# Kernel tuning notes

Measured on AMD Instinct MI355X. Metric: run time of the kernel, lower is better.

## Reference

```python
import jax, jax.numpy as jnp
import numpy as np

N_NODES = 100000
IN_DIM = 500
HID_DIM = 128
OUT_DIM = 40
N_EDGES = 1600000


def setup_inputs() -> dict:
    key = jax.random.key(0)
    k1, k2, k3, k4, k5 = jax.random.split(key, 5)
    x = jax.random.normal(k1, (N_NODES, IN_DIM), dtype=jnp.float32)
    edge_index = jax.random.randint(k2, (2, N_EDGES), 0, N_NODES, dtype=jnp.int64)
    # Glorot-style init for linear weights, zero bias (as in PyG GCNConv)
    W1 = jax.random.normal(k3, (IN_DIM, HID_DIM), dtype=jnp.float32) / np.sqrt(IN_DIM)
    b1 = jnp.zeros((HID_DIM,), dtype=jnp.float32)
    W2 = jax.random.normal(k4, (HID_DIM, OUT_DIM), dtype=jnp.float32) / np.sqrt(HID_DIM)
    b2 = jnp.zeros((OUT_DIM,), dtype=jnp.float32)
    return {"x": x, "edge_index": edge_index, "W1": W1, "b1": b1, "W2": W2, "b2": b2}


def reference(x, edge_index, W1, b1, W2, b2):
    N = x.shape[0]
    # GCNConv: add self-loops, symmetric normalization deg^-1/2 A deg^-1/2
    loops = jnp.arange(N, dtype=edge_index.dtype)
    src = jnp.concatenate([edge_index[0], loops])  # [E+N]
    dst = jnp.concatenate([edge_index[1], loops])  # [E+N]
    deg = jax.ops.segment_sum(jnp.ones_like(dst, dtype=x.dtype), dst, num_segments=N)
    dinv = jnp.where(deg > 0, jax.lax.rsqrt(deg), 0.0)
    norm = (dinv[src] * dinv[dst])[:, None]  # [E+N, 1]

    def gcn_conv(h, W, b):
        h = h @ W                              # [N, F_out] linear first (PyG order)
        msg = h[src] * norm                    # gather + scale: [E+N, F_out]
        agg = jax.ops.segment_sum(msg, dst, num_segments=N)  # scatter-add
        return agg + b

    h = jax.nn.relu(gcn_conv(x, W1, b1))
    # dropout(p=0.5) is identity in eval mode
    h = gcn_conv(h, W2, b2)
    return jax.nn.log_softmax(h, axis=1)
```

## Files before the change

### kernel.cpp

```cpp
#include <hip/hip_runtime.h>
#include <hip/hip_bf16.h>

#define IN_DIM 500
#define HID 128
#define OUTD 40
#define KPAD 512

typedef __bf16 bf16x8 __attribute__((ext_vector_type(8)));
typedef float f32x16 __attribute__((ext_vector_type(16)));

static __device__ __forceinline__ float rsqrt_acc(float x) {
  float r = rsqrtf(x);
  return r * (1.5f - 0.5f * x * r * r);
}

static __device__ __forceinline__ unsigned short bf16_of(float f) {
  __bf16 h = (__bf16)f;
  return __builtin_bit_cast(unsigned short, h);
}
static __device__ __forceinline__ float bf16_back(unsigned short u) {
  return (float)__builtin_bit_cast(__bf16, u);
}

__global__ void zero_kernel(int* __restrict__ p, int n) {
  int i = blockIdx.x * 256 + threadIdx.x;
  if (i < n) p[i] = 0;
}

__global__ void hist_kernel(const int* __restrict__ dst, int* __restrict__ deg, int E) {
  int e = blockIdx.x * 256 + threadIdx.x;
  if (e < E) atomicAdd(&deg[dst[e]], 1);
}

__global__ void dinv_kernel(const int* __restrict__ deg, float* __restrict__ dinv, int N) {
  int n = blockIdx.x * 256 + threadIdx.x;
  if (n < N) dinv[n] = rsqrt_acc((float)deg[n] + 1.0f);
}

__global__ void scan_a(const int* __restrict__ deg, int* __restrict__ partial,
                       int* __restrict__ blockSums, int N) {
  __shared__ int sums[256];
  int t = threadIdx.x;
  int base = blockIdx.x * 1024 + t * 4;
  int v0 = (base + 0) < N ? deg[base + 0] : 0;
  int v1 = (base + 1) < N ? deg[base + 1] : 0;
  int v2 = (base + 2) < N ? deg[base + 2] : 0;
  int v3 = (base + 3) < N ? deg[base + 3] : 0;
  int l0 = v0, l1 = l0 + v1, l2 = l1 + v2, l3 = l2 + v3;
  sums[t] = l3;
  __syncthreads();
  for (int o = 1; o < 256; o <<= 1) {
    int a = sums[t];
    int b = (t >= o) ? sums[t - o] : 0;
    __syncthreads();
    sums[t] = a + b;
    __syncthreads();
  }
  int excl = sums[t] - l3;
  if (t == 0) blockSums[blockIdx.x] = sums[255];
  if (base + 0 < N) partial[base + 0] = excl;
  if (base + 1 < N) partial[base + 1] = excl + l0;
  if (base + 2 < N) partial[base + 2] = excl + l1;
  if (base + 3 < N) partial[base + 3] = excl + l2;
}

__global__ void scan_b(int* __restrict__ blockSums, int nb) {
  __shared__ int s[256];
  int t = threadIdx.x;
  int orig = (t < nb) ? blockSums[t] : 0;
  s[t] = orig;
  __syncthreads();
  for (int o = 1; o < 256; o <<= 1) {
    int a = s[t];
    int b = (t >= o) ? s[t - o] : 0;
    __syncthreads();
    s[t] = a + b;
    __syncthreads();
  }
  if (t < nb) blockSums[t] = s[t] - orig;
}

__global__ void scan_c(int* __restrict__ row_ptr, const int* __restrict__ blockOff,
                       int* __restrict__ cursor, int N, int E) {
  int n = blockIdx.x * 256 + threadIdx.x;
  if (n < N) {
    int v = row_ptr[n] + blockOff[n >> 10];
    row_ptr[n] = v;
    cursor[n] = v;
  }
  if (n == 0 && blockIdx.x == 0) row_ptr[N] = E;
}

__global__ void place_kernel(const int* __restrict__ src, const int* __restrict__ dst,
                             const float* __restrict__ dinv, int* __restrict__ cursor,
                             int* __restrict__ eSrc, float* __restrict__ eW, int E) {
  int e = blockIdx.x * 256 + threadIdx.x;
  if (e < E) {
    int s = src[e], d = dst[e];
    int pos = atomicAdd(&cursor[d], 1);
    eSrc[pos] = s;
    eW[pos] = dinv[s] * dinv[d];
  }
}

__global__ void convW1_kernel(const float* __restrict__ W1, unsigned short* __restrict__ Whi,
                              unsigned short* __restrict__ Wlo) {
  int idx = blockIdx.x * 256 + threadIdx.x;
  if (idx >= HID * KPAD) return;
  int n = idx >> 9, k = idx & (KPAD - 1);
  float f = (k < IN_DIM) ? W1[(size_t)k * HID + n] : 0.f;
  unsigned short h = bf16_of(f);
  Whi[idx] = h;
  Wlo[idx] = bf16_of(f - bf16_back(h));
}

#define LSTR 40
__global__ __launch_bounds__(256) void gemm1_kernel(const float* __restrict__ X,
                                                    const unsigned short* __restrict__ Whi,
                                                    const unsigned short* __restrict__ Wlo,
                                                    float* __restrict__ H1, int N) {
  __shared__ unsigned short sAhi[128 * LSTR];
  __shared__ unsigned short sAlo[128 * LSTR];
  __shared__ unsigned short sBhi[128 * LSTR];
  __shared__ unsigned short sBlo[128 * LSTR];
  const int t = threadIdx.x;
  const int rowBase = blockIdx.x * 128;
  const int lane = t & 63;
  const int w = t >> 6;
  const int m = lane & 31;
  const int quad = lane >> 5;

  f32x16 acc[4];
#pragma unroll
  for (int i = 0; i < 4; i++) acc[i] = (f32x16)(0.f);

  const int srow = t >> 1;
  const int skoff = (t & 1) * 16;
  const bool rok = (rowBase + srow) < N;
  const float* xrow = X + (size_t)(rowBase + (rok ? srow : 0)) * IN_DIM;

  for (int k0 = 0; k0 < KPAD; k0 += 32) {
    __syncthreads();
    {
      float f[16];
      if (rok && (k0 + skoff + 16) <= IN_DIM) {
        const float4* p = (const float4*)(xrow + k0 + skoff);
        float4 v0 = p[0], v1 = p[1], v2 = p[2], v3 = p[3];
        f[0]=v0.x; f[1]=v0.y; f[2]=v0.z; f[3]=v0.w;
        f[4]=v1.x; f[5]=v1.y; f[6]=v1.z; f[7]=v1.w;
        f[8]=v2.x; f[9]=v2.y; f[10]=v2.z; f[11]=v2.w;
        f[12]=v3.x; f[13]=v3.y; f[14]=v3.z; f[15]=v3.w;
      } else {
#pragma unroll
        for (int j = 0; j < 16; j++) {
          int k = k0 + skoff + j;
          f[j] = (rok && k < IN_DIM) ? xrow[k] : 0.f;
        }
      }
#pragma unroll
      for (int g = 0; g < 4; g++) {
        ushort4 h, l;
        h.x = bf16_of(f[g*4+0]); l.x = bf16_of(f[g*4+0] - bf16_back(h.x));
        h.y = bf16_of(f[g*4+1]); l.y = bf16_of(f[g*4+1] - bf16_back(h.y));
        h.z = bf16_of(f[g*4+2]); l.z = bf16_of(f[g*4+2] - bf16_back(h.z));
        h.w = bf16_of(f[g*4+3]); l.w = bf16_of(f[g*4+3] - bf16_back(h.w));
        *(ushort4*)&sAhi[srow * LSTR + skoff + g * 4] = h;
        *(ushort4*)&sAlo[srow * LSTR + skoff + g * 4] = l;
      }
    }
    {
      const int n = srow;
      const size_t gb = (size_t)n * KPAD + k0 + skoff;
      uint4 h0 = *(const uint4*)&Whi[gb];
      uint4 h1v = *(const uint4*)&Whi[gb + 8];
      uint4 l0 = *(const uint4*)&Wlo[gb];
      uint4 l1 = *(const uint4*)&Wlo[gb + 8];
      *(uint4*)&sBhi[n * LSTR + skoff] = h0;
      *(uint4*)&sBhi[n * LSTR + skoff + 8] = h1v;
      *(uint4*)&sBlo[n * LSTR + skoff] = l0;
      *(uint4*)&sBlo[n * LSTR + skoff + 8] = l1;
    }
    __syncthreads();

#pragma unroll
    for (int sub = 0; sub < 2; sub++) {
      const int ks = sub * 16 + quad * 8;
      bf16x8 ah = *(const bf16x8*)&sAhi[(w * 32 + m) * LSTR + ks];
      bf16x8 al = *(const bf16x8*)&sAlo[(w * 32 + m) * LSTR + ks];
#pragma unroll
      for (int nt = 0; nt < 4; nt++) {
        bf16x8 bh = *(const bf16x8*)&sBhi[(nt * 32 + m) * LSTR + ks];
        bf16x8 bl = *(const bf16x8*)&sBlo[(nt * 32 + m) * LSTR + ks];
        acc[nt] = __builtin_amdgcn_mfma_f32_32x32x16_bf16(ah, bh, acc[nt], 0, 0, 0);
        acc[nt] = __builtin_amdgcn_mfma_f32_32x32x16_bf16(ah, bl, acc[nt], 0, 0, 0);
        acc[nt] = __builtin_amdgcn_mfma_f32_32x32x16_bf16(al, bh, acc[nt], 0, 0, 0);
      }
    }
  }

#pragma unroll
  for (int nt = 0; nt < 4; nt++) {
#pragma unroll
    for (int r = 0; r < 16; r++) {
      int rowin = (r & 3) + 8 * (r >> 2) + 4 * quad;
      int grow = rowBase + w * 32 + rowin;
      if (grow < N) H1[(size_t)grow * HID + nt * 32 + m] = acc[nt][r];
    }
  }
}

__global__ void agg1_kernel(const float* __restrict__ h1, const int* __restrict__ row_ptr,
                            const int* __restrict__ eSrc, const float* __restrict__ eW,
                            const float* __restrict__ dinv, const float* __restrict__ b1,
                            float* __restrict__ hrelu, int N) {
  int gid = blockIdx.x * 256 + threadIdx.x;
  int n = gid >> 5, c4 = (gid & 31) * 4;
  if (n >= N) return;
  float di = dinv[n];
  float sl = di * di;
  float4 acc = *(const float4*)&h1[(size_t)n * HID + c4];
  acc.x *= sl; acc.y *= sl; acc.z *= sl; acc.w *= sl;
  int i = row_ptr[n];
  const int s1 = row_ptr[n + 1];
  for (; i + 4 <= s1; i += 4) {
    int j0 = eSrc[i], j1 = eSrc[i + 1], j2 = eSrc[i + 2], j3 = eSrc[i + 3];
    float w0 = eW[i], w1 = eW[i + 1], w2 = eW[i + 2], w3 = eW[i + 3];
    float4 v0 = *(const float4*)&h1[(size_t)j0 * HID + c4];
    float4 v1 = *(const float4*)&h1[(size_t)j1 * HID + c4];
    float4 v2 = *(const float4*)&h1[(size_t)j2 * HID + c4];
    float4 v3 = *(const float4*)&h1[(size_t)j3 * HID + c4];
    acc.x += w0 * v0.x + w1 * v1.x + w2 * v2.x + w3 * v3.x;
    acc.y += w0 * v0.y + w1 * v1.y + w2 * v2.y + w3 * v3.y;
    acc.z += w0 * v0.z + w1 * v1.z + w2 * v2.z + w3 * v3.z;
    acc.w += w0 * v0.w + w1 * v1.w + w2 * v2.w + w3 * v3.w;
  }
  for (; i < s1; i++) {
    int j = eSrc[i];
    float w = eW[i];
    float4 v = *(const float4*)&h1[(size_t)j * HID + c4];
    acc.x += w * v.x; acc.y += w * v.y; acc.z += w * v.z; acc.w += w * v.w;
  }
  float4 bb = *(const float4*)&b1[c4];
  float4 r;
  r.x = fmaxf(acc.x + bb.x, 0.f);
  r.y = fmaxf(acc.y + bb.y, 0.f);
  r.z = fmaxf(acc.z + bb.z, 0.f);
  r.w = fmaxf(acc.w + bb.w, 0.f);
  *(float4*)&hrelu[(size_t)n * HID + c4] = r;
}

__global__ __launch_bounds__(256) void gemm2_kernel(const float* __restrict__ A,
                                                    const float* __restrict__ W2,
                                                    float* __restrict__ H2, int N) {
  __shared__ float tA[64 * 129];
  __shared__ float w2s[128 * 48];
  const int t = threadIdx.x;
  const int rowBase = blockIdx.x * 64;
  for (int idx = t; idx < 128 * 48; idx += 256) {
    int k = idx / 48, c = idx - k * 48;
    w2s[idx] = (c < OUTD) ? W2[k * OUTD + c] : 0.f;
  }
  for (int f = t; f < 2048; f += 256) {
    int row = f >> 5, c4 = (f & 31) * 4;
    float4 v = make_float4(0.f, 0.f, 0.f, 0.f);
    if (rowBase + row < N) v = *(const float4*)&A[(size_t)(rowBase + row) * HID + c4];
    tA[row * 129 + c4 + 0] = v.x;
    tA[row * 129 + c4 + 1] = v.y;
    tA[row * 129 + c4 + 2] = v.z;
    tA[row * 129 + c4 + 3] = v.w;
  }
  __syncthreads();
  const int row = t >> 2;
  const int c0 = (t & 3) * 12;
  float acc[12];
#pragma unroll
  for (int j = 0; j < 12; j++) acc[j] = 0.f;
  for (int k = 0; k < HID; k++) {
    float a = tA[row * 129 + k];
    const float* bp = &w2s[k * 48 + c0];
#pragma unroll
    for (int j = 0; j < 12; j++) acc[j] += a * bp[j];
  }
  int r = rowBase + row;
  if (r < N) {
#pragma unroll
    for (int j = 0; j < 12; j++) {
      int c = c0 + j;
      if (c < OUTD) H2[(size_t)r * OUTD + c] = acc[j];
    }
  }
}

__global__ void agg2_kernel(const float* __restrict__ h2, const int* __restrict__ row_ptr,
                            const int* __restrict__ eSrc, const float* __restrict__ eW,
                            const float* __restrict__ dinv, const float* __restrict__ b2,
                            float* __restrict__ out, int N) {
  int gid = blockIdx.x * 256 + threadIdx.x;
  int n = gid / 10;
  int c4 = (gid - n * 10) * 4;
  if (n >= N) return;
  float di = dinv[n];
  float sl = di * di;
  float4 acc = *(const float4*)&h2[(size_t)n * OUTD + c4];
  acc.x *= sl; acc.y *= sl; acc.z *= sl; acc.w *= sl;
  int i = row_ptr[n];
  const int s1 = row_ptr[n + 1];
  for (; i + 4 <= s1; i += 4) {
    int j0 = eSrc[i], j1 = eSrc[i + 1], j2 = eSrc[i + 2], j3 = eSrc[i + 3];
    float w0 = eW[i], w1 = eW[i + 1], w2 = eW[i + 2], w3 = eW[i + 3];
    float4 v0 = *(const float4*)&h2[(size_t)j0 * OUTD + c4];
    float4 v1 = *(const float4*)&h2[(size_t)j1 * OUTD + c4];
    float4 v2 = *(const float4*)&h2[(size_t)j2 * OUTD + c4];
    float4 v3 = *(const float4*)&h2[(size_t)j3 * OUTD + c4];
    acc.x += w0 * v0.x + w1 * v1.x + w2 * v2.x + w3 * v3.x;
    acc.y += w0 * v0.y + w1 * v1.y + w2 * v2.y + w3 * v3.y;
    acc.z += w0 * v0.z + w1 * v1.z + w2 * v2.z + w3 * v3.z;
    acc.w += w0 * v0.w + w1 * v1.w + w2 * v2.w + w3 * v3.w;
  }
  for (; i < s1; i++) {
    int j = eSrc[i];
    float w = eW[i];
    float4 v = *(const float4*)&h2[(size_t)j * OUTD + c4];
    acc.x += w * v.x; acc.y += w * v.y; acc.z += w * v.z; acc.w += w * v.w;
  }
  float* o = &out[(size_t)n * OUTD + c4];
  o[0] = acc.x + b2[c4 + 0];
  o[1] = acc.y + b2[c4 + 1];
  o[2] = acc.z + b2[c4 + 2];
  o[3] = acc.w + b2[c4 + 3];
}

__global__ void lsm_kernel(float* __restrict__ out, int N) {
  int n = blockIdx.x * 256 + threadIdx.x;
  if (n >= N) return;
  float* row = out + (size_t)n * OUTD;
  float v[OUTD];
  float m = -3.4e38f;
#pragma unroll
  for (int j = 0; j < OUTD; j++) {
    v[j] = row[j];
    m = fmaxf(m, v[j]);
  }
  float s = 0.f;
#pragma unroll
  for (int j = 0; j < OUTD; j++) s += expf(v[j] - m);
  float lse = m + logf(s);
#pragma unroll
  for (int j = 0; j < OUTD; j++) row[j] = v[j] - lse;
}

extern "C" void kernel_launch(void* const* d_in, const int* in_sizes, int n_in,
                              void* d_out, int out_size, void* d_ws, size_t ws_size,
                              hipStream_t stream) {
  const float* x  = (const float*)d_in[0];
  const int*   ei = (const int*)d_in[1];
  const float* W1 = (const float*)d_in[2];
  const float* b1 = (const float*)d_in[3];
  const float* W2 = (const float*)d_in[4];
  const float* b2 = (const float*)d_in[5];
  float* out = (float*)d_out;

  const int N = in_sizes[0] / IN_DIM;
  const int E = in_sizes[1] / 2;
  const int* src = ei;
  const int* dst = ei + E;

  char* wsb = (char*)d_ws;
  size_t off = 0;
  auto alloc = [&](size_t bytes) -> char* {
    char* p = wsb + off;
    off = (off + bytes + 1023) & ~(size_t)1023;
    return p;
  };
  int*   deg       = (int*)alloc((size_t)N * 4);
  float* dinv      = (float*)alloc((size_t)N * 4);
  int*   blockSums = (int*)alloc(1024);
  int*   row_ptr   = (int*)alloc((size_t)(N + 1) * 4);
  int*   cursor    = (int*)alloc((size_t)N * 4);
  int*   eSrc      = (int*)alloc((size_t)E * 4);
  float* eW        = (float*)alloc((size_t)E * 4);
  unsigned short* Whi = (unsigned short*)alloc((size_t)HID * KPAD * 2);
  unsigned short* Wlo = (unsigned short*)alloc((size_t)HID * KPAD * 2);
  float* h1        = (float*)alloc((size_t)N * HID * 4);
  float* hrelu     = (float*)alloc((size_t)N * HID * 4);
  float* h2        = h1;
  (void)n_in; (void)out_size;

  if (off > ws_size) return;

  const int gE = (E + 255) / 256;
  const int gN = (N + 255) / 256;
  const int nb = (N + 1023) / 1024;

  zero_kernel<<<gN, 256, 0, stream>>>(deg, N);
  hist_kernel<<<gE, 256, 0, stream>>>(dst, deg, E);
  dinv_kernel<<<gN, 256, 0, stream>>>(deg, dinv, N);
  scan_a<<<nb, 256, 0, stream>>>(deg, row_ptr, blockSums, N);
  scan_b<<<1, 256, 0, stream>>>(blockSums, nb);
  scan_c<<<gN, 256, 0, stream>>>(row_ptr, blockSums, cursor, N, E);
  place_kernel<<<gE, 256, 0, stream>>>(src, dst, dinv, cursor, eSrc, eW, E);
  convW1_kernel<<<(HID * KPAD + 255) / 256, 256, 0, stream>>>(W1, Whi, Wlo);

  gemm1_kernel<<<(N + 127) / 128, 256, 0, stream>>>(x, Whi, Wlo, h1, N);
  agg1_kernel<<<(N * 32 + 255) / 256, 256, 0, stream>>>(h1, row_ptr, eSrc, eW, dinv, b1, hrelu, N);
  gemm2_kernel<<<(N + 63) / 64, 256, 0, stream>>>(hrelu, W2, h2, N);
  agg2_kernel<<<(N * 10 + 255) / 256, 256, 0, stream>>>(h2, row_ptr, eSrc, eW, dinv, b2, out, N);
  lsm_kernel<<<gN, 256, 0, stream>>>(out, N);
}
```

Before: 763.9 us.

## Prefetch next GEMM1 k-tile into registers and pack edge src/weight pairs

The first-layer GEMM now loads the next 32-wide k-slice of X and W into registers while MFMAs run on the current shared-memory tile. It uses manual barriers that wait only on LDS (lgkmcnt), so global loads stay in flight across the barrier. Separately, the CSR edge source index and normalisation weight are interleaved into one int2 array, so each edge needs one 8-byte load instead of two separate loads in both aggregation kernels. The prefetch costs more registers, which may lower occupancy.

```diff
diff --git a/kernel.cpp b/kernel.cpp
--- a/kernel.cpp
+++ b/kernel.cpp
@@ -93,13 +93,15 @@
 
 __global__ void place_kernel(const int* __restrict__ src, const int* __restrict__ dst,
                              const float* __restrict__ dinv, int* __restrict__ cursor,
-                             int* __restrict__ eSrc, float* __restrict__ eW, int E) {
+                             int2* __restrict__ ePair, int E) {
   int e = blockIdx.x * 256 + threadIdx.x;
   if (e < E) {
     int s = src[e], d = dst[e];
     int pos = atomicAdd(&cursor[d], 1);
-    eSrc[pos] = s;
-    eW[pos] = dinv[s] * dinv[d];
+    int2 rec;
+    rec.x = s;
+    rec.y = __float_as_int(dinv[s] * dinv[d]);
+    ePair[pos] = rec;
   }
 }
 
@@ -115,6 +117,77 @@
 }
 
 #define LSTR 40
+
+#define G1_BAR() do { asm volatile("s_waitcnt lgkmcnt(0)" ::: "memory"); \
+                      __builtin_amdgcn_s_barrier(); } while (0)
+
+static __device__ __forceinline__ void g1_load(const float* __restrict__ xrow, bool rok,
+                                               const unsigned short* __restrict__ Whi,
+                                               const unsigned short* __restrict__ Wlo,
+                                               int srow, int skoff, int k0,
+                                               float (&f)[16], uint4 (&bhv)[2], uint4 (&blv)[2]) {
+  if (rok && (k0 + skoff + 16) <= IN_DIM) {
+    const float4* p = (const float4*)(xrow + k0 + skoff);
+    float4 v0 = p[0], v1 = p[1], v2 = p[2], v3 = p[3];
+    f[0]=v0.x; f[1]=v0.y; f[2]=v0.z; f[3]=v0.w;
+    f[4]=v1.x; f[5]=v1.y; f[6]=v1.z; f[7]=v1.w;
+    f[8]=v2.x; f[9]=v2.y; f[10]=v2.z; f[11]=v2.w;
+    f[12]=v3.x; f[13]=v3.y; f[14]=v3.z; f[15]=v3.w;
+  } else {
+#pragma unroll
+    for (int j = 0; j < 16; j++) {
+      int k = k0 + skoff + j;
+      f[j] = (rok && k < IN_DIM) ? xrow[k] : 0.f;
+    }
+  }
+  const size_t gb = (size_t)srow * KPAD + k0 + skoff;
+  bhv[0] = *(const uint4*)&Whi[gb];
+  bhv[1] = *(const uint4*)&Whi[gb + 8];
+  blv[0] = *(const uint4*)&Wlo[gb];
+  blv[1] = *(const uint4*)&Wlo[gb + 8];
+}
+
+static __device__ __forceinline__ void g1_stage(unsigned short* sAhi, unsigned short* sAlo,
+                                                unsigned short* sBhi, unsigned short* sBlo,
+                                                int srow, int skoff, const float (&f)[16],
+                                                const uint4 (&bhv)[2], const uint4 (&blv)[2]) {
+#pragma unroll
+  for (int g = 0; g < 4; g++) {
+    ushort4 h, l;
+    h.x = bf16_of(f[g*4+0]); l.x = bf16_of(f[g*4+0] - bf16_back(h.x));
+    h.y = bf16_of(f[g*4+1]); l.y = bf16_of(f[g*4+1] - bf16_back(h.y));
+    h.z = bf16_of(f[g*4+2]); l.z = bf16_of(f[g*4+2] - bf16_back(h.z));
+    h.w = bf16_of(f[g*4+3]); l.w = bf16_of(f[g*4+3] - bf16_back(h.w));
+    *(ushort4*)&sAhi[srow * LSTR + skoff + g * 4] = h;
+    *(ushort4*)&sAlo[srow * LSTR + skoff + g * 4] = l;
+  }
+  *(uint4*)&sBhi[srow * LSTR + skoff] = bhv[0];
+  *(uint4*)&sBhi[srow * LSTR + skoff + 8] = bhv[1];
+  *(uint4*)&sBlo[srow * LSTR + skoff] = blv[0];
+  *(uint4*)&sBlo[srow * LSTR + skoff + 8] = blv[1];
+}
+
+static __device__ __forceinline__ void g1_compute(const unsigned short* sAhi,
+                                                  const unsigned short* sAlo,
+                                                  const unsigned short* sBhi,
+                                                  const unsigned short* sBlo,
+                                                  int w, int m, int quad, f32x16 (&acc)[4]) {
+#pragma unroll
+  for (int sub = 0; sub < 2; sub++) {
+    const int ks = sub * 16 + quad * 8;
+    bf16x8 ah = *(const bf16x8*)&sAhi[(w * 32 + m) * LSTR + ks];
+    bf16x8 al = *(const bf16x8*)&sAlo[(w * 32 + m) * LSTR + ks];
+#pragma unroll
+    for (int nt = 0; nt < 4; nt++) {
+      bf16x8 bh = *(const bf16x8*)&sBhi[(nt * 32 + m) * LSTR + ks];
+      bf16x8 bl = *(const bf16x8*)&sBlo[(nt * 32 + m) * LSTR + ks];
+      acc[nt] = __builtin_amdgcn_mfma_f32_32x32x16_bf16(ah, bh, acc[nt], 0, 0, 0);
+      acc[nt] = __builtin_amdgcn_mfma_f32_32x32x16_bf16(ah, bl, acc[nt], 0, 0, 0);
+      acc[nt] = __builtin_amdgcn_mfma_f32_32x32x16_bf16(al, bh, acc[nt], 0, 0, 0);
+    }
+  }
+}
+
 __global__ __launch_bounds__(256) void gemm1_kernel(const float* __restrict__ X,
                                                     const unsigned short* __restrict__ Whi,
                                                     const unsigned short* __restrict__ Wlo,
@@ -139,63 +212,23 @@
   const bool rok = (rowBase + srow) < N;
   const float* xrow = X + (size_t)(rowBase + (rok ? srow : 0)) * IN_DIM;
 
-  for (int k0 = 0; k0 < KPAD; k0 += 32) {
-    __syncthreads();
-    {
-      float f[16];
-      if (rok && (k0 + skoff + 16) <= IN_DIM) {
-        const float4* p = (const float4*)(xrow + k0 + skoff);
-        float4 v0 = p[0], v1 = p[1], v2 = p[2], v3 = p[3];
-        f[0]=v0.x; f[1]=v0.y; f[2]=v0.z; f[3]=v0.w;
-        f[4]=v1.x; f[5]=v1.y; f[6]=v1.z; f[7]=v1.w;
-        f[8]=v2.x; f[9]=v2.y; f[10]=v2.z; f[11]=v2.w;
-        f[12]=v3.x; f[13]=v3.y; f[14]=v3.z; f[15]=v3.w;
-      } else {
-#pragma unroll
-        for (int j = 0; j < 16; j++) {
-          int k = k0 + skoff + j;
-          f[j] = (rok && k < IN_DIM) ? xrow[k] : 0.f;
-        }
-      }
-#pragma unroll
-      for (int g = 0; g < 4; g++) {
-        ushort4 h, l;
-        h.x = bf16_of(f[g*4+0]); l.x = bf16_of(f[g*4+0] - bf16_back(h.x));
-        h.y = bf16_of(f[g*4+1]); l.y = bf16_of(f[g*4+1] - bf16_back(h.y));
-        h.z = bf16_of(f[g*4+2]); l.z = bf16_of(f[g*4+2] - bf16_back(h.z));
-        h.w = bf16_of(f[g*4+3]); l.w = bf16_of(f[g*4+3] - bf16_back(h.w));
-        *(ushort4*)&sAhi[srow * LSTR + skoff + g * 4] = h;
-        *(ushort4*)&sAlo[srow * LSTR + skoff + g * 4] = l;
-      }
-    }
-    {
-      const int n = srow;
-      const size_t gb = (size_t)n * KPAD + k0 + skoff;
-      uint4 h0 = *(const uint4*)&Whi[gb];
-      uint4 h1v = *(const uint4*)&Whi[gb + 8];
-      uint4 l0 = *(const uint4*)&Wlo[gb];
-      uint4 l1 = *(const uint4*)&Wlo[gb + 8];
-      *(uint4*)&sBhi[n * LSTR + skoff] = h0;
-      *(uint4*)&sBhi[n * LSTR + skoff + 8] = h1v;
-      *(uint4*)&sBlo[n * LSTR + skoff] = l0;
-      *(uint4*)&sBlo[n * LSTR + skoff + 8] = l1;
-    }
-    __syncthreads();
-
-#pragma unroll
-    for (int sub = 0; sub < 2; sub++) {
-      const int ks = sub * 16 + quad * 8;
-      bf16x8 ah = *(const bf16x8*)&sAhi[(w * 32 + m) * LSTR + ks];
-      bf16x8 al = *(const bf16x8*)&sAlo[(w * 32 + m) * LSTR + ks];
-#pragma unroll
-      for (int nt = 0; nt < 4; nt++) {
-        bf16x8 bh = *(const bf16x8*)&sBhi[(nt * 32 + m) * LSTR + ks];
-        bf16x8 bl = *(const bf16x8*)&sBlo[(nt * 32 + m) * LSTR + ks];
-        acc[nt] = __builtin_amdgcn_mfma_f32_32x32x16_bf16(ah, bh, acc[nt], 0, 0, 0);
-        acc[nt] = __builtin_amdgcn_mfma_f32_32x32x16_bf16(ah, bl, acc[nt], 0, 0, 0);
-        acc[nt] = __builtin_amdgcn_mfma_f32_32x32x16_bf16(al, bh, acc[nt], 0, 0, 0);
-      }
-    }
+  float fA[16]; uint4 bhA[2], blA[2];
+  float fB[16]; uint4 bhB[2], blB[2];
+  g1_load(xrow, rok, Whi, Wlo, srow, skoff, 0, fA, bhA, blA);
+
+#pragma unroll 1
+  for (int r = 0; r < 16; r += 2) {
+    g1_stage(sAhi, sAlo, sBhi, sBlo, srow, skoff, fA, bhA, blA);
+    G1_BAR();
+    g1_load(xrow, rok, Whi, Wlo, srow, skoff, (r + 1) * 32, fB, bhB, blB);
+    g1_compute(sAhi, sAlo, sBhi, sBlo, w, m, quad, acc);
+    G1_BAR();
+
+    g1_stage(sAhi, sAlo, sBhi, sBlo, srow, skoff, fB, bhB, blB);
+    G1_BAR();
+    if (r + 2 < 16) g1_load(xrow, rok, Whi, Wlo, srow, skoff, (r + 2) * 32, fA, bhA, blA);
+    g1_compute(sAhi, sAlo, sBhi, sBlo, w, m, quad, acc);
+    G1_BAR();
   }
 
 #pragma unroll
@@ -210,9 +243,8 @@
 }
 
 __global__ void agg1_kernel(const float* __restrict__ h1, const int* __restrict__ row_ptr,
-                            const int* __restrict__ eSrc, const float* __restrict__ eW,
-                            const float* __restrict__ dinv, const float* __restrict__ b1,
-                            float* __restrict__ hrelu, int N) {
+                            const int2* __restrict__ ePair, const float* __restrict__ dinv,
+                            const float* __restrict__ b1, float* __restrict__ hrelu, int N) {
   int gid = blockIdx.x * 256 + threadIdx.x;
   int n = gid >> 5, c4 = (gid & 31) * 4;
   if (n >= N) return;
@@ -223,21 +255,22 @@
   int i = row_ptr[n];
   const int s1 = row_ptr[n + 1];
   for (; i + 4 <= s1; i += 4) {
-    int j0 = eSrc[i], j1 = eSrc[i + 1], j2 = eSrc[i + 2], j3 = eSrc[i + 3];
-    float w0 = eW[i], w1 = eW[i + 1], w2 = eW[i + 2], w3 = eW[i + 3];
-    float4 v0 = *(const float4*)&h1[(size_t)j0 * HID + c4];
-    float4 v1 = *(const float4*)&h1[(size_t)j1 * HID + c4];
-    float4 v2 = *(const float4*)&h1[(size_t)j2 * HID + c4];
-    float4 v3 = *(const float4*)&h1[(size_t)j3 * HID + c4];
+    int2 e0 = ePair[i], e1 = ePair[i + 1], e2 = ePair[i + 2], e3 = ePair[i + 3];
+    float w0 = __int_as_float(e0.y), w1 = __int_as_float(e1.y);
+    float w2 = __int_as_float(e2.y), w3 = __int_as_float(e3.y);
+    float4 v0 = *(const float4*)&h1[(size_t)e0.x * HID + c4];
+    float4 v1 = *(const float4*)&h1[(size_t)e1.x * HID + c4];
+    float4 v2 = *(const float4*)&h1[(size_t)e2.x * HID + c4];
+    float4 v3 = *(const float4*)&h1[(size_t)e3.x * HID + c4];
     acc.x += w0 * v0.x + w1 * v1.x + w2 * v2.x + w3 * v3.x;
     acc.y += w0 * v0.y + w1 * v1.y + w2 * v2.y + w3 * v3.y;
     acc.z += w0 * v0.z + w1 * v1.z + w2 * v2.z + w3 * v3.z;
     acc.w += w0 * v0.w + w1 * v1.w + w2 * v2.w + w3 * v3.w;
   }
   for (; i < s1; i++) {
-    int j = eSrc[i];
-    float w = eW[i];
-    float4 v = *(const float4*)&h1[(size_t)j * HID + c4];
+    int2 e = ePair[i];
+    float w = __int_as_float(e.y);
+    float4 v = *(const float4*)&h1[(size_t)e.x * HID + c4];
     acc.x += w * v.x; acc.y += w * v.y; acc.z += w * v.z; acc.w += w * v.w;
   }
   float4 bb = *(const float4*)&b1[c4];
@@ -292,9 +325,8 @@
 }
 
 __global__ void agg2_kernel(const float* __restrict__ h2, const int* __restrict__ row_ptr,
-                            const int* __restrict__ eSrc, const float* __restrict__ eW,
-                            const float* __restrict__ dinv, const float* __restrict__ b2,
-                            float* __restrict__ out, int N) {
+                            const int2* __restrict__ ePair, const float* __restrict__ dinv,
+                            const float* __restrict__ b2, float* __restrict__ out, int N) {
   int gid = blockIdx.x * 256 + threadIdx.x;
   int n = gid / 10;
   int c4 = (gid - n * 10) * 4;
@@ -306,21 +338,22 @@
   int i = row_ptr[n];
   const int s1 = row_ptr[n + 1];
   for (; i + 4 <= s1; i += 4) {
-    int j0 = eSrc[i], j1 = eSrc[i + 1], j2 = eSrc[i + 2], j3 = eSrc[i + 3];
-    float w0 = eW[i], w1 = eW[i + 1], w2 = eW[i + 2], w3 = eW[i + 3];
-    float4 v0 = *(const float4*)&h2[(size_t)j0 * OUTD + c4];
-    float4 v1 = *(const float4*)&h2[(size_t)j1 * OUTD + c4];
-    float4 v2 = *(const float4*)&h2[(size_t)j2 * OUTD + c4];
-    float4 v3 = *(const float4*)&h2[(size_t)j3 * OUTD + c4];
+    int2 e0 = ePair[i], e1 = ePair[i + 1], e2 = ePair[i + 2], e3 = ePair[i + 3];
+    float w0 = __int_as_float(e0.y), w1 = __int_as_float(e1.y);
+    float w2 = __int_as_float(e2.y), w3 = __int_as_float(e3.y);
+    float4 v0 = *(const float4*)&h2[(size_t)e0.x * OUTD + c4];
+    float4 v1 = *(const float4*)&h2[(size_t)e1.x * OUTD + c4];
+    float4 v2 = *(const float4*)&h2[(size_t)e2.x * OUTD + c4];
+    float4 v3 = *(const float4*)&h2[(size_t)e3.x * OUTD + c4];
     acc.x += w0 * v0.x + w1 * v1.x + w2 * v2.x + w3 * v3.x;
     acc.y += w0 * v0.y + w1 * v1.y + w2 * v2.y + w3 * v3.y;
     acc.z += w0 * v0.z + w1 * v1.z + w2 * v2.z + w3 * v3.z;
     acc.w += w0 * v0.w + w1 * v1.w + w2 * v2.w + w3 * v3.w;
   }
   for (; i < s1; i++) {
-    int j = eSrc[i];
-    float w = eW[i];
-    float4 v = *(const float4*)&h2[(size_t)j * OUTD + c4];
+    int2 e = ePair[i];
+    float w = __int_as_float(e.y);
+    float4 v = *(const float4*)&h2[(size_t)e.x * OUTD + c4];
     acc.x += w * v.x; acc.y += w * v.y; acc.z += w * v.z; acc.w += w * v.w;
   }
   float* o = &out[(size_t)n * OUTD + c4];
@@ -377,8 +410,7 @@
   int*   blockSums = (int*)alloc(1024);
   int*   row_ptr   = (int*)alloc((size_t)(N + 1) * 4);
   int*   cursor    = (int*)alloc((size_t)N * 4);
-  int*   eSrc      = (int*)alloc((size_t)E * 4);
-  float* eW        = (float*)alloc((size_t)E * 4);
+  int2*  ePair     = (int2*)alloc((size_t)E * 8);
   unsigned short* Whi = (unsigned short*)alloc((size_t)HID * KPAD * 2);
   unsigned short* Wlo = (unsigned short*)alloc((size_t)HID * KPAD * 2);
   float* h1        = (float*)alloc((size_t)N * HID * 4);
@@ -398,12 +430,12 @@
   scan_a<<<nb, 256, 0, stream>>>(deg, row_ptr, blockSums, N);
   scan_b<<<1, 256, 0, stream>>>(blockSums, nb);
   scan_c<<<gN, 256, 0, stream>>>(row_ptr, blockSums, cursor, N, E);
-  place_kernel<<<gE, 256, 0, stream>>>(src, dst, dinv, cursor, eSrc, eW, E);
+  place_kernel<<<gE, 256, 0, stream>>>(src, dst, dinv, cursor, ePair, E);
   convW1_kernel<<<(HID * KPAD + 255) / 256, 256, 0, stream>>>(W1, Whi, Wlo);
 
   gemm1_kernel<<<(N + 127) / 128, 256, 0, stream>>>(x, Whi, Wlo, h1, N);
-  agg1_kernel<<<(N * 32 + 255) / 256, 256, 0, stream>>>(h1, row_ptr, eSrc, eW, dinv, b1, hrelu, N);
+  agg1_kernel<<<(N * 32 + 255) / 256, 256, 0, stream>>>(h1, row_ptr, ePair, dinv, b1, hrelu, N);
   gemm2_kernel<<<(N + 63) / 64, 256, 0, stream>>>(hrelu, W2, h2, N);
-  agg2_kernel<<<(N * 10 + 255) / 256, 256, 0, stream>>>(h2, row_ptr, eSrc, eW, dinv, b2, out, N);
+  agg2_kernel<<<(N * 10 + 255) / 256, 256, 0, stream>>>(h2, row_ptr, ePair, dinv, b2, out, N);
   lsm_kernel<<<gN, 256, 0, stream>>>(out, N);
 }
```

After: 747.3 us. 1.02x faster.
